# Kernel optimization log

Measured on AMD Instinct MI355X. Metric: run time of the kernel, lower is better.

Reference implementation:

```python
import jax, jax.numpy as jnp
import numpy as np

D_MODEL = 1024
NUM_HEADS = 16
HEAD_DIM = D_MODEL // NUM_HEADS
B, S = 2, 2048


def setup_inputs() -> dict:
    key = jax.random.key(0)
    ks = jax.random.split(key, 8)
    scale = 1.0 / np.sqrt(D_MODEL)
    inp = {
        "query": jax.random.normal(ks[0], (B, S, D_MODEL), jnp.float32),
        "key": jax.random.normal(ks[1], (B, S, D_MODEL), jnp.float32),
        "value": jax.random.normal(ks[2], (B, S, D_MODEL), jnp.float32),
        # causal mask, broadcastable over batch and heads
        "mask": jnp.tril(jnp.ones((S, S), dtype=bool))[None, None, :, :],
        # torch nn.Linear weights: y = x @ W.T (+ b)
        "Wq": jax.random.normal(ks[3], (D_MODEL, D_MODEL), jnp.float32) * scale,
        "Wk": jax.random.normal(ks[4], (D_MODEL, D_MODEL), jnp.float32) * scale,
        "Wv": jax.random.normal(ks[5], (D_MODEL, D_MODEL), jnp.float32) * scale,
        "Wo": jax.random.normal(ks[6], (D_MODEL, D_MODEL), jnp.float32) * scale,
        "bo": jax.random.normal(ks[7], (D_MODEL,), jnp.float32) * scale,
    }
    return inp


def _split_heads(x):
    b, s, _ = x.shape
    return x.reshape(b, s, NUM_HEADS, HEAD_DIM).transpose(0, 2, 1, 3)  # [B,H,S,Dh]


def reference(query, key, value, mask, Wq, Wk, Wv, Wo, bo):
    q = _split_heads(query @ Wq.T)
    k = _split_heads(key @ Wk.T)
    v = _split_heads(value @ Wv.T)
    scores = jnp.einsum("bhqd,bhkd->bhqk", q, k) / jnp.sqrt(jnp.float32(HEAD_DIM))
    scores = jnp.where(mask, scores, jnp.float32(-jnp.inf))
    attn = jax.nn.softmax(scores, axis=-1)
    out = jnp.einsum("bhqk,bhkd->bhqd", attn, v)  # [B,H,S,Dh]
    out = out.transpose(0, 2, 1, 3).reshape(query.shape[0], q.shape[2], D_MODEL)
    return out @ Wo.T + bo
```

## Files before the change

kernel.cpp:

```cpp
#include <hip/hip_runtime.h>
#include <hip/hip_bf16.h>

#define DM   1024
#define NH   16
#define HD   64
#define SEQ  2048
#define BATCH 2
#define MTOT (BATCH*SEQ)

typedef unsigned short u16;
typedef __attribute__((ext_vector_type(8))) short bf16x8;
typedef __attribute__((ext_vector_type(4))) float f32x4;

#define SC2F 0.1803368801111464f

__device__ __forceinline__ float bf2f(u16 h) {
  union { unsigned int i; float f; } u; u.i = ((unsigned int)h) << 16; return u.f;
}
__device__ __forceinline__ u16 f2bf(float f) {
  union { float f; unsigned int i; } u; u.f = f;
  unsigned int r = u.i + 0x7fffu + ((u.i >> 16) & 1u);
  return (u16)(r >> 16);
}
__device__ __forceinline__ unsigned int pk2(float lo, float hi) {
  union { float f; unsigned int u; } a, b; a.f = lo; b.f = hi;
  return ((a.u + 0x8000u) >> 16) | ((b.u + 0x8000u) & 0xFFFF0000u);
}
__device__ __forceinline__ unsigned int cvtpk(float lo, float hi) {
  unsigned int r;
  asm("v_cvt_pk_bf16_f32 %0, %1, %2" : "=v"(r) : "v"(lo), "v"(hi));
  return r;
}

__device__ __forceinline__ uint4 load8_bf16(const void* base, size_t elemOff, bool isf32) {
  if (!isf32) return *(const uint4*)((const u16*)base + elemOff);
  const float* f = (const float*)base + elemOff;
  f32x4 a = *(const f32x4*)f;
  f32x4 b = *(const f32x4*)(f + 4);
  union { u16 h[8]; uint4 v; } r;
  r.h[0]=f2bf(a[0]); r.h[1]=f2bf(a[1]); r.h[2]=f2bf(a[2]); r.h[3]=f2bf(a[3]);
  r.h[4]=f2bf(b[0]); r.h[5]=f2bf(b[1]); r.h[6]=f2bf(b[2]); r.h[7]=f2bf(b[3]);
  return r.v;
}

__global__ __launch_bounds__(256) void prep(
    const void* __restrict__ q, const void* __restrict__ k, const void* __restrict__ v,
    const void* __restrict__ wq, const void* __restrict__ wk, const void* __restrict__ wv,
    const void* __restrict__ wo, const void* __restrict__ bo,
    u16* __restrict__ Xq, u16* __restrict__ Xk, u16* __restrict__ Xv,
    u16* __restrict__ Wqb, u16* __restrict__ Wkb, u16* __restrict__ Wvb, u16* __restrict__ Wob,
    float* __restrict__ biasf, int* __restrict__ flag_out)
{
  const int tid = threadIdx.x;
  __shared__ int cnts[4];
  {
    const u16* qs = (const u16*)q;
    int e0 = (qs[tid*2]   >> 7) & 0xFF;
    int e1 = (qs[tid*2+1] >> 7) & 0xFF;
    int c = ((e0 >= 0x6E && e0 <= 0x8F) ? 1 : 0) + ((e1 >= 0x6E && e1 <= 0x8F) ? 1 : 0);
    c += __shfl_xor(c, 1);  c += __shfl_xor(c, 2);  c += __shfl_xor(c, 4);
    c += __shfl_xor(c, 8);  c += __shfl_xor(c, 16); c += __shfl_xor(c, 32);
    if ((tid & 63) == 0) cnts[tid >> 6] = c;
  }
  __syncthreads();
  const bool isf32 = (cnts[0] + cnts[1] + cnts[2] + cnts[3]) < 400;

  const int z = blockIdx.z;
  if (z == 7) {
    if (blockIdx.x == 0) {
      if (tid == 0) *flag_out = isf32 ? 0 : 1;
      for (int i = tid; i < DM; i += 256)
        biasf[i] = isf32 ? ((const float*)bo)[i] : bf2f(((const u16*)bo)[i]);
    }
    return;
  }
  const void* src; u16* dst; size_t n;
  switch (z) {
    case 0: src=q;  dst=Xq;  n=(size_t)MTOT*DM; break;
    case 1: src=k;  dst=Xk;  n=(size_t)MTOT*DM; break;
    case 2: src=v;  dst=Xv;  n=(size_t)MTOT*DM; break;
    case 3: src=wq; dst=Wqb; n=(size_t)DM*DM;   break;
    case 4: src=wk; dst=Wkb; n=(size_t)DM*DM;   break;
    case 5: src=wv; dst=Wvb; n=(size_t)DM*DM;   break;
    default: src=wo; dst=Wob; n=(size_t)DM*DM;  break;
  }
  const size_t stride = (size_t)gridDim.x * 256 * 8;
  for (size_t i = ((size_t)blockIdx.x * 256 + tid) * 8; i < n; i += stride)
    *(uint4*)(dst + i) = load8_bf16(src, i, isf32);
}

__device__ __forceinline__ void gld16(const u16* g, u16* l) {
  __builtin_amdgcn_global_load_lds(
      (const __attribute__((address_space(1))) void*)g,
      (__attribute__((address_space(3))) void*)l, 16, 0, 0);
}

__global__ __launch_bounds__(256) void gemm_qkv(
    const u16* __restrict__ X0, const u16* __restrict__ X1, const u16* __restrict__ X2,
    const u16* __restrict__ W0, const u16* __restrict__ W1, const u16* __restrict__ W2,
    u16* __restrict__ F0, u16* __restrict__ F1, u16* __restrict__ F2)
{
  __shared__ u16 As[128*32];
  __shared__ u16 Bs[128*32];

  const int zz = blockIdx.z;
  const u16* X = (zz==0) ? X0 : ((zz==1) ? X1 : X2);
  const u16* W = (zz==0) ? W0 : ((zz==1) ? W1 : W2);
  u16* outF    = (zz==0) ? F0 : ((zz==1) ? F1 : F2);

  const int tid = threadIdx.x;
  const int wave = tid >> 6, lane = tid & 63, quad = lane >> 4, l16 = lane & 15;
  const int wr = wave >> 1, wc = wave & 1;
  const int m0 = blockIdx.x * 128, n0 = blockIdx.y * 128;

  const int sg = ((lane & 3) ^ ((lane >> 3) & 3)) * 8;
  const int rS = wave*32 + (lane >> 2);
  const u16* gA0 = X + (size_t)(m0 + rS)*DM + sg;
  const u16* gA1 = X + (size_t)(m0 + rS + 16)*DM + sg;
  const u16* gB0 = W + (size_t)(n0 + rS)*DM + sg;
  const u16* gB1 = W + (size_t)(n0 + rS + 16)*DM + sg;
  u16* lA0 = &As[wave*1024];
  u16* lA1 = &As[wave*1024 + 512];
  u16* lB0 = &Bs[wave*1024];
  u16* lB1 = &Bs[wave*1024 + 512];

  const int xslot8 = (quad ^ ((l16 >> 1) & 3)) * 8;

  f32x4 acc[4][4];
#pragma unroll
  for (int i = 0; i < 4; i++)
#pragma unroll
    for (int j = 0; j < 4; j++) { acc[i][j][0]=0.f; acc[i][j][1]=0.f; acc[i][j][2]=0.f; acc[i][j][3]=0.f; }

  for (int k0 = 0; k0 < DM; k0 += 32) {
    __syncthreads();
    gld16(gA0 + k0, lA0);
    gld16(gA1 + k0, lA1);
    gld16(gB0 + k0, lB0);
    gld16(gB1 + k0, lB1);
    __syncthreads();

    bf16x8 af[4], bfr[4];
#pragma unroll
    for (int fr = 0; fr < 4; fr++)
      af[fr] = *(const bf16x8*)&As[(wr*64 + fr*16 + l16)*32 + xslot8];
#pragma unroll
    for (int fc = 0; fc < 4; fc++)
      bfr[fc] = *(const bf16x8*)&Bs[(wc*64 + fc*16 + l16)*32 + xslot8];
#pragma unroll
    for (int fr = 0; fr < 4; fr++)
#pragma unroll
      for (int fc = 0; fc < 4; fc++)
        acc[fr][fc] = __builtin_amdgcn_mfma_f32_16x16x32_bf16(af[fr], bfr[fc], acc[fr][fc], 0, 0, 0);
  }

  if (zz == 2) {
    __shared__ u16 Ts[64*128];
    const int bb = m0 >> 11;
    const int s0 = m0 & (SEQ-1);
#pragma unroll
    for (int p = 0; p < 2; p++) {
      __syncthreads();
      if (wc == p) {
#pragma unroll
        for (int fr = 0; fr < 4; fr++) {
#pragma unroll
          for (int fc = 0; fc < 4; fc++) {
            const int dl = fc*16 + l16;
            const int sb = wr*64 + fr*16 + quad*4;
            const int slot = (sb >> 3) ^ (dl & 15);
            u16* rowp = &Ts[dl*128 + slot*8 + (sb & 7)];
            *(unsigned int*)(rowp)     = pk2(acc[fr][fc][0], acc[fr][fc][1]);
            *(unsigned int*)(rowp + 2) = pk2(acc[fr][fc][2], acc[fr][fc][3]);
          }
        }
      }
      __syncthreads();
      const int dl2 = tid >> 2, ch4 = tid & 3;
      const int hh = (n0 + p*64) >> 6;
      u16* dst = outF + ((size_t)(bb*NH + hh)*HD + dl2)*SEQ + s0 + ch4*32;
#pragma unroll
      for (int j = 0; j < 4; j++) {
        const int c  = ch4*4 + j;
        const int lo = (c >> 2)*32 + (c & 3)*4;
        const int hi = lo + 16;
        uint2 lo2 = *(const uint2*)&Ts[dl2*128 + (((lo >> 3) ^ (dl2 & 15))*8) + (lo & 7)];
        uint2 hi2 = *(const uint2*)&Ts[dl2*128 + (((hi >> 3) ^ (dl2 & 15))*8) + (hi & 7)];
        uint4 o; o.x = lo2.x; o.y = lo2.y; o.z = hi2.x; o.w = hi2.y;
        *(uint4*)&dst[j*8] = o;
      }
    }
    return;
  }

#pragma unroll
  for (int fr = 0; fr < 4; fr++) {
#pragma unroll
    for (int rr = 0; rr < 4; rr++) {
      const int m = m0 + wr*64 + fr*16 + quad*4 + rr;
#pragma unroll
      for (int fc = 0; fc < 4; fc++) {
        const int n = n0 + wc*64 + fc*16 + l16;
        float vv = acc[fr][fc][rr];
        if (zz == 0) vv *= SC2F;
        const int b = m >> 11, s = m & (SEQ-1), h = n >> 6, d = n & (HD-1);
        outF[((size_t)(b*NH + h)*SEQ + s)*HD + d] = f2bf(vv);
      }
    }
  }
}

__global__ __launch_bounds__(256) void gemm_out(
    const u16* __restrict__ X, const u16* __restrict__ W,
    const float* __restrict__ biasf, void* __restrict__ outP,
    const int* __restrict__ dflag)
{
  __shared__ u16 As[128*32];
  __shared__ u16 Bs[64*32];

  const int tid = threadIdx.x;
  const int wave = tid >> 6, lane = tid & 63, quad = lane >> 4, l16 = lane & 15;
  const int wr = wave >> 1, wc = wave & 1;
  const int m0 = blockIdx.x * 128, n0 = blockIdx.y * 64;

  const int sg = ((lane & 3) ^ ((lane >> 3) & 3)) * 8;
  const int rA = wave*32 + (lane >> 2);
  const int rB = wave*16 + (lane >> 2);
  const u16* gA0 = X + (size_t)(m0 + rA)*DM + sg;
  const u16* gA1 = X + (size_t)(m0 + rA + 16)*DM + sg;
  const u16* gB0 = W + (size_t)(n0 + rB)*DM + sg;
  u16* lA0 = &As[wave*1024];
  u16* lA1 = &As[wave*1024 + 512];
  u16* lB0 = &Bs[wave*512];

  const int xslot8 = (quad ^ ((l16 >> 1) & 3)) * 8;

  f32x4 acc[4][2];
#pragma unroll
  for (int i = 0; i < 4; i++)
#pragma unroll
    for (int j = 0; j < 2; j++) { acc[i][j][0]=0.f; acc[i][j][1]=0.f; acc[i][j][2]=0.f; acc[i][j][3]=0.f; }

  for (int k0 = 0; k0 < DM; k0 += 32) {
    __syncthreads();
    gld16(gA0 + k0, lA0);
    gld16(gA1 + k0, lA1);
    gld16(gB0 + k0, lB0);
    __syncthreads();

    bf16x8 af[4], bfr[2];
#pragma unroll
    for (int fr = 0; fr < 4; fr++)
      af[fr] = *(const bf16x8*)&As[(wr*64 + fr*16 + l16)*32 + xslot8];
#pragma unroll
    for (int fc = 0; fc < 2; fc++)
      bfr[fc] = *(const bf16x8*)&Bs[(wc*32 + fc*16 + l16)*32 + xslot8];
#pragma unroll
    for (int fr = 0; fr < 4; fr++)
#pragma unroll
      for (int fc = 0; fc < 2; fc++)
        acc[fr][fc] = __builtin_amdgcn_mfma_f32_16x16x32_bf16(af[fr], bfr[fc], acc[fr][fc], 0, 0, 0);
  }

  const bool isf32 = (*dflag == 0);
#pragma unroll
  for (int fr = 0; fr < 4; fr++) {
#pragma unroll
    for (int rr = 0; rr < 4; rr++) {
      const int m = m0 + wr*64 + fr*16 + quad*4 + rr;
#pragma unroll
      for (int fc = 0; fc < 2; fc++) {
        const int n = n0 + wc*32 + fc*16 + l16;
        float vv = acc[fr][fc][rr] + biasf[n];
        if (isf32) ((float*)outP)[(size_t)m*DM + n] = vv;
        else       ((u16*)outP)[(size_t)m*DM + n]   = f2bf(vv);
      }
    }
  }
}

__global__ __launch_bounds__(256) void attn_mfma(
    const u16* __restrict__ Qb, const u16* __restrict__ Kb,
    const u16* __restrict__ Vtb,
    u16* __restrict__ Opart, float* __restrict__ mlpart)
{
  __shared__ u16 Ks[2][64*64];
  __shared__ u16 Vs[2][64*64];

  const int bh = blockIdx.x;
  const int pr = blockIdx.y, z = blockIdx.z;
  const u16* Qp = Qb  + (size_t)bh * SEQ * HD;
  const u16* Kp = Kb  + (size_t)bh * SEQ * HD;
  const u16* Vp = Vtb + (size_t)bh * HD * SEQ;

  const int tid  = threadIdx.x;
  const int wave = tid >> 6, lane = tid & 63, quad = lane >> 4, l16 = lane & 15;

  const int i0 = wave*128 + lane, i1 = i0 + 64;
  const int r0 = i0 >> 3, c0 = (i0 & 7) ^ (r0 & 7);
  const int r1 = i1 >> 3, c1 = (i1 & 7) ^ (r1 & 7);
  const int kq_off0 = r0*HD + c0*8;
  const int kq_off1 = r1*HD + c1*8;
  const int v_off0  = r0*SEQ + c0*8;
  const int v_off1  = r1*SEQ + c1*8;

  const int l7 = l16 & 7;
  const int ql = wave*16 + l16;
  const int so = wave*1024;

  for (int ph = 0; ph < 2; ph++) {
    const int qt = ph ? (31 - pr) : pr;
    const int n = qt + 1, half = (n + 1) >> 1;
    const int klo = z ? half : 0, khi = z ? n : half;
    const int q0 = qt * 64;
    const int qg = q0 + ql;

    const u16* qrow = Qp + (size_t)qg * HD;
    const bf16x8 bq0 = *(const bf16x8*)(qrow + quad*8);
    const bf16x8 bq1 = *(const bf16x8*)(qrow + 32 + quad*8);

    f32x4 O[4];
#pragma unroll
    for (int u = 0; u < 4; u++) { O[u][0]=0.f; O[u][1]=0.f; O[u][2]=0.f; O[u][3]=0.f; }
    float mi = -__builtin_inff(), li = 0.f;

    if (klo < khi) {
      gld16(Kp + klo*(64*HD) + kq_off0, &Ks[0][so]);
      gld16(Kp + klo*(64*HD) + kq_off1, &Ks[0][so + 512]);
      gld16(Vp + klo*64 + v_off0, &Vs[0][so]);
      gld16(Vp + klo*64 + v_off1, &Vs[0][so + 512]);
    }
    asm volatile("" ::: "memory");

    for (int kt = klo; kt < khi; kt++) {
      const int cb = (kt - klo) & 1;
      const u16* kb = &Ks[cb][0];
      const u16* vb = &Vs[cb][0];
      if (kt + 1 < khi) {
        u16* kn = &Ks[cb ^ 1][so];
        u16* vn = &Vs[cb ^ 1][so];
        gld16(Kp + (kt+1)*(64*HD) + kq_off0, kn);
        gld16(Kp + (kt+1)*(64*HD) + kq_off1, kn + 512);
        gld16(Vp + (kt+1)*64 + v_off0, vn);
        gld16(Vp + (kt+1)*64 + v_off1, vn + 512);
        asm volatile("s_waitcnt vmcnt(4)" ::: "memory");
      } else {
        asm volatile("s_waitcnt vmcnt(0)" ::: "memory");
      }
      __builtin_amdgcn_s_barrier();
      asm volatile("" ::: "memory");

      f32x4 st[4];
#pragma unroll
      for (int t = 0; t < 4; t++) { st[t][0]=0.f; st[t][1]=0.f; st[t][2]=0.f; st[t][3]=0.f; }
#pragma unroll
      for (int s = 0; s < 2; s++) {
        const bf16x8 bq = s ? bq1 : bq0;
        const int ch = s*4 + quad;
#pragma unroll
        for (int t = 0; t < 4; t++) {
          bf16x8 ak = *(const bf16x8*)&kb[((t*16 + l16)*8 + (ch ^ l7))*8];
          st[t] = __builtin_amdgcn_mfma_f32_16x16x32_bf16(ak, bq, st[t], 0, 0, 0);
        }
      }

      if (kt == qt) {
#pragma unroll
        for (int t = 0; t < 4; t++)
#pragma unroll
          for (int r = 0; r < 4; r++)
            if (kt*64 + t*16 + quad*4 + r > qg) st[t][r] = -__builtin_inff();
      }

      float a0 = fmaxf(fmaxf(st[0][0], st[0][1]), fmaxf(st[0][2], st[0][3]));
      float a1 = fmaxf(fmaxf(st[1][0], st[1][1]), fmaxf(st[1][2], st[1][3]));
      float a2 = fmaxf(fmaxf(st[2][0], st[2][1]), fmaxf(st[2][2], st[2][3]));
      float a3 = fmaxf(fmaxf(st[3][0], st[3][1]), fmaxf(st[3][2], st[3][3]));
      float mx = fmaxf(fmaxf(a0, a1), fmaxf(a2, a3));
      mx = fmaxf(mx, __shfl_xor(mx, 16));
      mx = fmaxf(mx, __shfl_xor(mx, 32));
      const float nm = fmaxf(mi, mx);
      const float al = exp2f(mi - nm);
      unsigned int w[4][2];
      float ps = 0.f;
#pragma unroll
      for (int t = 0; t < 4; t++) {
        float p0 = exp2f(st[t][0] - nm), p1 = exp2f(st[t][1] - nm);
        float p2 = exp2f(st[t][2] - nm), p3 = exp2f(st[t][3] - nm);
        ps += (p0 + p1) + (p2 + p3);
        w[t][0] = cvtpk(p0, p1);
        w[t][1] = cvtpk(p2, p3);
      }
      li = li * al + ps;
      mi = nm;
#pragma unroll
      for (int u = 0; u < 4; u++) {
        O[u][0] *= al; O[u][1] *= al; O[u][2] *= al; O[u][3] *= al;
      }

#pragma unroll
      for (int s = 0; s < 2; s++) {
        union { unsigned int u[4]; bf16x8 v; } bp;
        bp.u[0] = w[2*s][0];   bp.u[1] = w[2*s][1];
        bp.u[2] = w[2*s+1][0]; bp.u[3] = w[2*s+1][1];
        const int ch = s*4 + quad;
#pragma unroll
        for (int u = 0; u < 4; u++) {
          bf16x8 av = *(const bf16x8*)&vb[((u*16 + l16)*8 + (ch ^ l7))*8];
          O[u] = __builtin_amdgcn_mfma_f32_16x16x32_bf16(av, bp.v, O[u], 0, 0, 0);
        }
      }

      asm volatile("" ::: "memory");
      __builtin_amdgcn_s_barrier();
      asm volatile("" ::: "memory");
    }

    li += __shfl_xor(li, 16);
    li += __shfl_xor(li, 32);

    const int pi = (bh*32 + qt)*2 + z;
    u16* op = Opart + (size_t)pi*4096 + ql*64;
#pragma unroll
    for (int u = 0; u < 4; u++) {
      uint2 u2; u2.x = pk2(O[u][0], O[u][1]); u2.y = pk2(O[u][2], O[u][3]);
      *(uint2*)&op[u*16 + quad*4] = u2;
    }
    if (quad == 0) {
      float2 ml2; ml2.x = mi; ml2.y = li;
      *(float2*)&mlpart[(size_t)pi*128 + ql*2] = ml2;
    }
  }
}

__global__ __launch_bounds__(64) void attn_merge(
    const u16* __restrict__ Opart, const float* __restrict__ mlpart,
    u16* __restrict__ aO)
{
  const int g = blockIdx.x;
  const int bh = g & 31, qt = g >> 5;
  const int b = bh >> 4, h = bh & 15;
  const int t = threadIdx.x;
  const int pi0 = (bh*32 + qt)*2, pi1 = pi0 + 1;

  const float2 ml0 = *(const float2*)&mlpart[(size_t)pi0*128 + t*2];
  const float2 ml1 = *(const float2*)&mlpart[(size_t)pi1*128 + t*2];
  const float M = fmaxf(ml0.x, ml1.x);
  float w0 = exp2f(ml0.x - M), w1 = exp2f(ml1.x - M);
  const float inv = 1.0f / (w0*ml0.y + w1*ml1.y);
  w0 *= inv; w1 *= inv;

  const u16* o0 = Opart + (size_t)pi0*4096 + t*64;
  const u16* o1 = Opart + (size_t)pi1*4096 + t*64;
  u16* out = aO + (size_t)(b*SEQ + qt*64 + t)*DM + h*HD;
#pragma unroll
  for (int d0 = 0; d0 < 64; d0 += 8) {
    union { uint4 v; u16 h[8]; } a, c; union { uint4 v; u16 h[8]; } bb;
    a.v  = *(const uint4*)&o0[d0];
    bb.v = *(const uint4*)&o1[d0];
#pragma unroll
    for (int j = 0; j < 8; j += 2) {
      float x0 = w0*bf2f(a.h[j])   + w1*bf2f(bb.h[j]);
      float x1 = w0*bf2f(a.h[j+1]) + w1*bf2f(bb.h[j+1]);
      unsigned int pk = pk2(x0, x1);
      c.h[j] = (u16)(pk & 0xFFFF); c.h[j+1] = (u16)(pk >> 16);
    }
    *(uint4*)&out[d0] = c.v;
  }
}

extern "C" void kernel_launch(void* const* d_in, const int* in_sizes, int n_in,
                              void* d_out, int out_size, void* d_ws, size_t ws_size,
                              hipStream_t stream) {
  const void* q  = d_in[0];
  const void* k  = d_in[1];
  const void* v  = d_in[2];
  const void* wq = d_in[4];
  const void* wk = d_in[5];
  const void* wv = d_in[6];
  const void* wo = d_in[7];
  const void* bo = d_in[8];

  const size_t TX = (size_t)MTOT*DM;
  const size_t TW = (size_t)DM*DM;
  u16* ws  = (u16*)d_ws;
  u16* Xq  = ws;
  u16* Xk  = ws + TX;
  u16* Xv  = ws + 2*TX;
  u16* Wqb = ws + 3*TX;
  u16* Wkb = Wqb + TW;
  u16* Wvb = Wqb + 2*TW;
  u16* Wob = Wqb + 3*TW;
  u16* Qw  = ws + 3*TX + 4*TW;
  u16* Kw  = Qw + TX;
  u16* Vt  = Qw + 2*TX;
  u16*   Opart  = Xk;
  float* mlpart = (float*)Wqb;
  u16*   aO     = Xq;
  float* biasf  = (float*)(Qw + 3*TX);
  int*   fl     = (int*)(biasf + DM);

  dim3 blk(256);
  prep<<<dim3(512, 1, 8), blk, 0, stream>>>(q, k, v, wq, wk, wv, wo, bo,
      Xq, Xk, Xv, Wqb, Wkb, Wvb, Wob, biasf, fl);
  gemm_qkv<<<dim3(MTOT/128, DM/128, 3), blk, 0, stream>>>(
      Xq, Xk, Xv, Wqb, Wkb, Wvb, Qw, Kw, Vt);
  attn_mfma<<<dim3(BATCH*NH, 16, 2), blk, 0, stream>>>(Qw, Kw, Vt, Opart, mlpart);
  attn_merge<<<dim3(32*32), dim3(64), 0, stream>>>(Opart, mlpart, aO);
  gemm_out<<<dim3(MTOT/128, DM/64), blk, 0, stream>>>(aO, Wob, biasf, d_out, fl);
}
```

Measured before the change: 240.0 us.

## Double-buffer LDS tiles in QKV and output GEMMs with async prefetch

Both projection GEMMs now use two LDS buffers per operand, issuing the global-to-LDS loads for the next K tile before computing on the current one. Manual vmcnt waits and raw barriers replace the pair of __syncthreads per iteration, so global memory latency can overlap the MFMA work. The cost is double the LDS footprint, which may lower occupancy. It also relies on hand-counted waitcnt values matching the loads actually issued.

```diff
diff --git a/kernel.cpp b/kernel.cpp
--- a/kernel.cpp
+++ b/kernel.cpp
@@ -100,8 +100,11 @@
     const u16* __restrict__ W0, const u16* __restrict__ W1, const u16* __restrict__ W2,
     u16* __restrict__ F0, u16* __restrict__ F1, u16* __restrict__ F2)
 {
-  __shared__ u16 As[128*32];
-  __shared__ u16 Bs[128*32];
+  __shared__ __align__(16) u16 smem[16384];
+  u16* const A0 = smem;
+  u16* const A1 = smem + 4096;
+  u16* const B0 = smem + 8192;
+  u16* const B1 = smem + 12288;
 
   const int zz = blockIdx.z;
   const u16* X = (zz==0) ? X0 : ((zz==1) ? X1 : X2);
@@ -119,10 +122,7 @@
   const u16* gA1 = X + (size_t)(m0 + rS + 16)*DM + sg;
   const u16* gB0 = W + (size_t)(n0 + rS)*DM + sg;
   const u16* gB1 = W + (size_t)(n0 + rS + 16)*DM + sg;
-  u16* lA0 = &As[wave*1024];
-  u16* lA1 = &As[wave*1024 + 512];
-  u16* lB0 = &Bs[wave*1024];
-  u16* lB1 = &Bs[wave*1024 + 512];
+  const int so = wave*1024;
 
   const int xslot8 = (quad ^ ((l16 >> 1) & 3)) * 8;
 
@@ -132,30 +132,50 @@
 #pragma unroll
     for (int j = 0; j < 4; j++) { acc[i][j][0]=0.f; acc[i][j][1]=0.f; acc[i][j][2]=0.f; acc[i][j][3]=0.f; }
 
+  gld16(gA0, A0 + so);
+  gld16(gA1, A0 + so + 512);
+  gld16(gB0, B0 + so);
+  gld16(gB1, B0 + so + 512);
+  asm volatile("" ::: "memory");
+
   for (int k0 = 0; k0 < DM; k0 += 32) {
-    __syncthreads();
-    gld16(gA0 + k0, lA0);
-    gld16(gA1 + k0, lA1);
-    gld16(gB0 + k0, lB0);
-    gld16(gB1 + k0, lB1);
-    __syncthreads();
+    const int cb = (k0 >> 5) & 1;
+    u16* const Ab = cb ? A1 : A0;
+    u16* const Bb = cb ? B1 : B0;
+    if (k0 + 32 < DM) {
+      u16* const An = cb ? A0 : A1;
+      u16* const Bn = cb ? B0 : B1;
+      gld16(gA0 + k0 + 32, An + so);
+      gld16(gA1 + k0 + 32, An + so + 512);
+      gld16(gB0 + k0 + 32, Bn + so);
+      gld16(gB1 + k0 + 32, Bn + so + 512);
+      asm volatile("s_waitcnt vmcnt(4)" ::: "memory");
+    } else {
+      asm volatile("s_waitcnt vmcnt(0)" ::: "memory");
+    }
+    __builtin_amdgcn_s_barrier();
+    asm volatile("" ::: "memory");
 
     bf16x8 af[4], bfr[4];
 #pragma unroll
     for (int fr = 0; fr < 4; fr++)
-      af[fr] = *(const bf16x8*)&As[(wr*64 + fr*16 + l16)*32 + xslot8];
+      af[fr] = *(const bf16x8*)&Ab[(wr*64 + fr*16 + l16)*32 + xslot8];
 #pragma unroll
     for (int fc = 0; fc < 4; fc++)
-      bfr[fc] = *(const bf16x8*)&Bs[(wc*64 + fc*16 + l16)*32 + xslot8];
+      bfr[fc] = *(const bf16x8*)&Bb[(wc*64 + fc*16 + l16)*32 + xslot8];
 #pragma unroll
     for (int fr = 0; fr < 4; fr++)
 #pragma unroll
       for (int fc = 0; fc < 4; fc++)
         acc[fr][fc] = __builtin_amdgcn_mfma_f32_16x16x32_bf16(af[fr], bfr[fc], acc[fr][fc], 0, 0, 0);
+
+    asm volatile("" ::: "memory");
+    __builtin_amdgcn_s_barrier();
+    asm volatile("" ::: "memory");
   }
 
   if (zz == 2) {
-    __shared__ u16 Ts[64*128];
+    u16* const Ts = smem;
     const int bb = m0 >> 11;
     const int s0 = m0 & (SEQ-1);
 #pragma unroll
@@ -215,8 +235,11 @@
     const float* __restrict__ biasf, void* __restrict__ outP,
     const int* __restrict__ dflag)
 {
-  __shared__ u16 As[128*32];
-  __shared__ u16 Bs[64*32];
+  __shared__ __align__(16) u16 smem[12288];
+  u16* const A0 = smem;
+  u16* const A1 = smem + 4096;
+  u16* const B0 = smem + 8192;
+  u16* const B1 = smem + 10240;
 
   const int tid = threadIdx.x;
   const int wave = tid >> 6, lane = tid & 63, quad = lane >> 4, l16 = lane & 15;
@@ -229,9 +252,7 @@
   const u16* gA0 = X + (size_t)(m0 + rA)*DM + sg;
   const u16* gA1 = X + (size_t)(m0 + rA + 16)*DM + sg;
   const u16* gB0 = W + (size_t)(n0 + rB)*DM + sg;
-  u16* lA0 = &As[wave*1024];
-  u16* lA1 = &As[wave*1024 + 512];
-  u16* lB0 = &Bs[wave*512];
+  const int soA = wave*1024, soB = wave*512;
 
   const int xslot8 = (quad ^ ((l16 >> 1) & 3)) * 8;
 
@@ -241,25 +262,44 @@
 #pragma unroll
     for (int j = 0; j < 2; j++) { acc[i][j][0]=0.f; acc[i][j][1]=0.f; acc[i][j][2]=0.f; acc[i][j][3]=0.f; }
 
+  gld16(gA0, A0 + soA);
+  gld16(gA1, A0 + soA + 512);
+  gld16(gB0, B0 + soB);
+  asm volatile("" ::: "memory");
+
   for (int k0 = 0; k0 < DM; k0 += 32) {
-    __syncthreads();
-    gld16(gA0 + k0, lA0);
-    gld16(gA1 + k0, lA1);
-    gld16(gB0 + k0, lB0);
-    __syncthreads();
+    const int cb = (k0 >> 5) & 1;
+    u16* const Ab = cb ? A1 : A0;
+    u16* const Bb = cb ? B1 : B0;
+    if (k0 + 32 < DM) {
+      u16* const An = cb ? A0 : A1;
+      u16* const Bn = cb ? B0 : B1;
+      gld16(gA0 + k0 + 32, An + soA);
+      gld16(gA1 + k0 + 32, An + soA + 512);
+      gld16(gB0 + k0 + 32, Bn + soB);
+      asm volatile("s_waitcnt vmcnt(3)" ::: "memory");
+    } else {
+      asm volatile("s_waitcnt vmcnt(0)" ::: "memory");
+    }
+    __builtin_amdgcn_s_barrier();
+    asm volatile("" ::: "memory");
 
     bf16x8 af[4], bfr[2];
 #pragma unroll
     for (int fr = 0; fr < 4; fr++)
-      af[fr] = *(const bf16x8*)&As[(wr*64 + fr*16 + l16)*32 + xslot8];
+      af[fr] = *(const bf16x8*)&Ab[(wr*64 + fr*16 + l16)*32 + xslot8];
 #pragma unroll
     for (int fc = 0; fc < 2; fc++)
-      bfr[fc] = *(const bf16x8*)&Bs[(wc*32 + fc*16 + l16)*32 + xslot8];
+      bfr[fc] = *(const bf16x8*)&Bb[(wc*32 + fc*16 + l16)*32 + xslot8];
 #pragma unroll
     for (int fr = 0; fr < 4; fr++)
 #pragma unroll
       for (int fc = 0; fc < 2; fc++)
         acc[fr][fc] = __builtin_amdgcn_mfma_f32_16x16x32_bf16(af[fr], bfr[fc], acc[fr][fc], 0, 0, 0);
+
+    asm volatile("" ::: "memory");
+    __builtin_amdgcn_s_barrier();
+    asm volatile("" ::: "memory");
   }
 
   const bool isf32 = (*dflag == 0);
```

After: 231.5 us. -3.5%, faster.
